# Performance work log

Hardware: AMD Instinct MI355X
Metric: run time of the kernel (lower is better)

The kernel has to match this reference:

```python
import jax, jax.numpy as jnp
import numpy as np

NUM_CLASS = 20
STRIDE = 4.0
B, H, W, G, NV = 8, 128, 128, 64, 40


def setup_inputs() -> dict:
    key = jax.random.key(0)
    ks = jax.random.split(key, 8)
    keypoints = jax.random.normal(ks[0], (B, H, W, NUM_CLASS), jnp.float32)
    preg = jax.random.uniform(ks[1], (B, H, W, 4), jnp.float32, 1.0, 40.0)
    fpn = jax.random.normal(ks[2], (B, H, W, NUM_CLASS), jnp.float32)
    masks = jnp.ones((B, H, W, G), jnp.float32)
    scalar_y = jax.random.uniform(ks[3], (B, G), jnp.float32, 5.0, 25.0)
    scalar_x = jax.random.uniform(ks[4], (B, G), jnp.float32, 5.0, 25.0)
    # ground truth: [cy, cx, y1, x1, y2, x2, class]; rows >= NV are zero padding
    rng = np.random.default_rng(0)
    gt = np.zeros((B, G, 7), np.float32)
    cy = rng.uniform(20.0, 492.0, (B, NV)).astype(np.float32)
    cx = rng.uniform(20.0, 492.0, (B, NV)).astype(np.float32)
    hh = rng.uniform(16.0, 120.0, (B, NV)).astype(np.float32)
    ww = rng.uniform(16.0, 120.0, (B, NV)).astype(np.float32)
    gt[:, :NV, 0] = cy
    gt[:, :NV, 1] = cx
    gt[:, :NV, 2] = np.clip(cy - hh / 2, 1.0, 510.0)
    gt[:, :NV, 3] = np.clip(cx - ww / 2, 1.0, 510.0)
    gt[:, :NV, 4] = np.clip(cy + hh / 2, 1.0, 510.0)
    gt[:, :NV, 5] = np.clip(cx + ww / 2, 1.0, 510.0)
    gt[:, :NV, 6] = rng.integers(1, NUM_CLASS + 1, (B, NV)).astype(np.float32)
    return {
        "keypoints": keypoints,
        "preg": preg,
        "fpn": fpn,
        "ground_truth": jnp.asarray(gt),
        "masks": masks,
        "scalar_y": scalar_y,
        "scalar_x": scalar_x,
    }


def _image_loss(gravity_pred, dist_pred, heatmap_pred, gt, masks, sy, sx):
    f32 = jnp.float32
    Hh, Ww, C = gravity_pred.shape
    Gg = gt.shape[0]
    # padding boundary: first row whose cy (col 0) is the minimum (==0 padding)
    slice_index = jnp.argmin(gt[:, 0])
    valid = jnp.arange(Gg) < slice_index
    vf = valid.astype(f32)

    gy = (gt[:, 0] + 0.5) / STRIDE
    gx = (gt[:, 1] + 0.5) / STRIDE
    by1 = (gt[:, 2] + 0.5) / STRIDE
    bx1 = (gt[:, 3] + 0.5) / STRIDE
    by2 = (gt[:, 4] + 0.5) / STRIDE
    bx2 = (gt[:, 5] + 0.5) / STRIDE
    cid = gt[:, 6].astype(jnp.int32) - 1
    kp_y = jnp.clip(jnp.floor(gt[:, 0] / STRIDE).astype(jnp.int32), 0, Hh - 1)
    kp_x = jnp.clip(jnp.floor(gt[:, 1] / STRIDE).astype(jnp.int32), 0, Ww - 1)

    grid_y = (jnp.arange(Hh, dtype=f32) + 0.5)[:, None, None]  # [H,1,1]
    grid_x = (jnp.arange(Ww, dtype=f32) + 0.5)[None, :, None]  # [1,W,1]

    dist_l = grid_x - bx1  # [1,W,G]
    dist_r = bx2 - grid_x
    dist_t = grid_y - by1  # [H,1,G]
    dist_b = by2 - grid_y
    ymask = (dist_t > 0.0).astype(f32) * (dist_b > 0.0).astype(f32)
    xmask = (dist_l > 0.0).astype(f32) * (dist_r > 0.0).astype(f32)
    heatmask = ymask * xmask * masks * vf  # [H,W,G]
    dist_l = dist_l * heatmask
    dist_r = dist_r * heatmask
    dist_t = dist_t * heatmask
    dist_b = dist_b * heatmask
    loc = jnp.max(heatmask, axis=-1)  # [H,W]
    dist_area = (dist_l + dist_r) * (dist_t + dist_b)
    area_pad = dist_area + (1.0 - heatmask) * 1e8
    area_min = jnp.min(area_pad, axis=-1, keepdims=True)
    dist_mask = (dist_area == area_min).astype(f32) * loc[..., None]  # [H,W,G]
    dl = jnp.max(dist_l * dist_mask, axis=-1)
    dr = jnp.max(dist_r * dist_mask, axis=-1)
    dt = jnp.max(dist_t * dist_mask, axis=-1)
    db = jnp.max(dist_b * dist_mask, axis=-1)

    pl, pr, pt, pb = (dist_pred[..., k] for k in range(4))
    inter = (jnp.minimum(dl, pl) + jnp.minimum(dr, pr)) * (jnp.minimum(dt, pt) + jnp.minimum(db, pb))
    union = (dl + dr) * (dt + db) + (pl + pr) * (pt + pb) - inter
    iou = inter / (union + 1e-12)

    red = jnp.exp(-(((grid_y - 0.5 - jnp.floor(gy)) / jnp.sqrt(sy)) ** 2
                    + ((grid_x - 0.5 - jnp.floor(gx)) / jnp.sqrt(sx)) ** 2) / 2.0) * vf  # [H,W,G]
    iou_red = jnp.max(red, axis=-1)
    iou_loss = jnp.sum(-jnp.log(iou + 1e-12) * loc * (iou_red * 4.0 + 1.0))

    # per-class max over gts of that class (== boolean_mask + reduce_max; empty -> 0)
    seg = jnp.where(valid & (cid >= 0) & (cid < C), cid, C)
    red_gt = jnp.maximum(jax.ops.segment_max(red.transpose(2, 0, 1), seg, num_segments=C + 1)[:C], 0.0).transpose(1, 2, 0)
    hm_gt = jnp.maximum(jax.ops.segment_max(dist_mask.transpose(2, 0, 1), seg, num_segments=C + 1)[:C], 0.0).transpose(1, 2, 0)
    gt_kp = jnp.zeros((Hh, Ww, C + 1), f32).at[kp_y, kp_x, seg].max(vf)[..., :C]

    sig, ls = jax.nn.sigmoid, jax.nn.log_sigmoid
    pos = -(1.0 - sig(gravity_pred)) ** 2 * ls(gravity_pred) * gt_kp
    neg = -(1.0 - red_gt) ** 4 * sig(gravity_pred) ** 2 * (-gravity_pred + ls(gravity_pred)) * (1.0 - gt_kp)
    gravity_loss = jnp.sum(pos) + jnp.sum(neg)

    hpos = -10.0 * (1.0 - sig(heatmap_pred)) ** 2 * ls(heatmap_pred) * hm_gt
    hneg = -10.0 * sig(heatmap_pred) ** 2 * (-heatmap_pred + ls(heatmap_pred)) * (1.0 - hm_gt)
    s_hg = jnp.sum(hm_gt)
    hm_loss = jnp.sum(hneg) / (jnp.asarray(Hh * Ww * C, f32) - s_hg)

    cond = s_hg != 0.0
    safe_hg = jnp.where(cond, s_hg, 1.0)
    s_loc = jnp.sum(loc)
    safe_loc = jnp.where(s_loc > 0.0, s_loc, 1.0)
    n_valid = jnp.maximum(slice_index.astype(f32), 1.0)
    hm2 = hm_loss + jnp.sum(hpos) / safe_hg
    iou_out = jnp.where(cond, iou_loss / safe_loc, 0.0)
    grav_out = jnp.where(cond, gravity_loss / n_valid, 0.0)
    hm_out = jnp.where(cond, hm2, hm_loss)
    total = jnp.where(cond, iou_out + grav_out + hm2, hm_loss)
    return iou_out, hm_out, grav_out, total


def reference(keypoints, preg, fpn, ground_truth, masks, scalar_y, scalar_x):
    losses = jax.vmap(_image_loss)(keypoints, preg, fpn, ground_truth, masks, scalar_y, scalar_x)
    # layer returns the mean total loss over the batch
    return jnp.mean(losses[3])
```

## Files before the change

### kernel.cpp

```cpp
#include <hip/hip_runtime.h>
#include <math.h>

#define Bc 8
#define Hc 128
#define Wc 128
#define Cc 20
#define Gc 64
#define HWc (Hc*Wc)
#define NBLK2 (Bc*HWc/128)

#define WS_STRIDE 768
#define OFF_BOX   0
#define OFF_RED   256
#define OFF_KPIX  512
#define OFF_SEG   576
#define OFF_START 640
#define WS_NV     704
#define WS_ACC    705
#define WS_SLICE  712

__global__ __launch_bounds__(64) void prep_kernel(
    const float* __restrict__ gt, const float* __restrict__ sy,
    const float* __restrict__ sx, float* __restrict__ ws)
{
  const int b = blockIdx.x;
  const int g = threadIdx.x;
  const float* row = gt + (size_t)(b*Gc + g)*7;
  const float cy = row[0];
  const float cx = row[1];

  float v = cy; int idx = g;
  #pragma unroll
  for (int o = 32; o > 0; o >>= 1) {
    const float ov = __shfl_down(v, o, 64);
    const int   oi = __shfl_down(idx, o, 64);
    if (ov < v || (ov == v && oi < idx)) { v = ov; idx = oi; }
  }
  const int slice = __shfl(idx, 0, 64);
  const bool valid = g < slice;
  const int cid = (int)row[6] - 1;
  const int cls = (cid >= 0 && cid < Cc) ? cid : Cc;

  __shared__ int counts[Cc+1], offs[Cc+1], starts[Cc+2];
  if (g < Cc+1) { counts[g] = 0; offs[g] = 0; }
  __syncthreads();
  if (valid) atomicAdd(&counts[cls], 1);
  __syncthreads();
  if (g == 0) {
    int acc = 0;
    for (int c = 0; c < Cc+1; ++c) { starts[c] = acc; acc += counts[c]; }
    starts[Cc+1] = acc;
  }
  __syncthreads();

  float* wb = ws + (size_t)b*WS_STRIDE;
  int*  wbi = (int*)wb;
  float4 bx;
  bx.x = (row[2]+0.5f)*0.25f;
  bx.y = (row[3]+0.5f)*0.25f;
  bx.z = (row[4]+0.5f)*0.25f;
  bx.w = (row[5]+0.5f)*0.25f;
  ((float4*)(wb + OFF_BOX))[g] = bx;
  wbi[OFF_SEG+g] = (valid && cls < Cc) ? cls : Cc;
  if (valid) {
    const int pos = starts[cls] + atomicAdd(&offs[cls], 1);
    float4 rp;
    rp.x = floorf((cy+0.5f)*0.25f);
    rp.y = floorf((cx+0.5f)*0.25f);
    rp.z = 0.5f / sy[b*Gc+g];
    rp.w = 0.5f / sx[b*Gc+g];
    ((float4*)(wb + OFF_RED))[pos] = rp;
    int kpy = (int)floorf(cy*0.25f); kpy = kpy < 0 ? 0 : (kpy > Hc-1 ? Hc-1 : kpy);
    int kpx = (int)floorf(cx*0.25f); kpx = kpx < 0 ? 0 : (kpx > Wc-1 ? Wc-1 : kpx);
    wbi[OFF_KPIX+pos] = kpy*Wc + kpx;
  }
  if (g < Cc+2) wbi[OFF_START+g] = starts[g];
  if (g == 0) { wb[WS_NV] = fmaxf((float)slice, 1.0f); wbi[WS_SLICE] = slice; }
  if (g < 6) wb[WS_ACC+g] = 0.0f;
}

__device__ __forceinline__ float wave_sum(float v) {
  #pragma unroll
  for (int o = 32; o > 0; o >>= 1) v += __shfl_down(v, o, 64);
  return v;
}

__global__ __launch_bounds__(256, 4) void main_kernel(
  const float* __restrict__ kpt, const float* __restrict__ preg,
  const float* __restrict__ fpn, const float* __restrict__ masks,
  const float* __restrict__ wsc, float* __restrict__ wsa)
{
  __shared__ float s_part[4][6];

  const int tid = threadIdx.x;
  const int wv = tid >> 6, ln = tid & 63;
  const int half = ln >> 5, sub = ln & 31;
  const int pi  = wv*32 + sub;
  const int pix = blockIdx.x*128 + pi;
  const int b   = blockIdx.x >> 7;
  const int hw  = pix & (HWc-1);
  const int h = hw >> 7, w = hw & (Wc-1);

  const float* wb  = wsc + (size_t)b*WS_STRIDE;
  const int*   wbi = (const int*)wb;
  const float4* __restrict__ box4 = (const float4*)(wb + OFF_BOX);
  const float4* __restrict__ red4 = (const float4*)(wb + OFF_RED);
  const int nslice = wbi[WS_SLICE];

  const float wx = w + 0.5f, hy = h + 0.5f;
  const float px_ = (float)w, py_ = (float)h;
  const float4* mrow4 = (const float4*)(masks + (size_t)pix*Gc);

  const float4 p4 = *(const float4*)(preg + (size_t)pix*4);
  const float4* kq4 = (const float4*)(kpt + (size_t)pix*Cc);
  const float4* fq4 = (const float4*)(fpn + (size_t)pix*Cc);
  const float4 kg0 = kq4[half], kg1 = kq4[2+half], kg2 = kq4[4];
  const float4 fg0 = fq4[half], fg1 = fq4[2+half], fg2 = fq4[4];

  float amin = 3.0e38f, loc = 0.f, mmin = 0.f; int gmin = 0;
  const int nC2 = (nslice + 7) >> 3;
  float4 mc0 = mrow4[half];
  float4 mc1 = mrow4[2 + half];
  for (int c2 = 0; c2 < nC2; ++c2) {
    const int pfci = 2*(c2+2) + half;
    const float4 mn = mrow4[pfci < 16 ? pfci : (14+half)];
    const int ci = 2*c2 + half;
    #pragma unroll
    for (int j = 0; j < 4; ++j) {
      const int g = ci*4 + j;
      const float m = (j==0)?mc0.x:(j==1)?mc0.y:(j==2)?mc0.z:mc0.w;
      const float4 bx = box4[g];
      const float dl = wx - bx.y, dr = bx.w - wx;
      const float dt = hy - bx.x, db = bx.z - hy;
      const bool inb = (dl > 0.f) & (dr > 0.f) & (dt > 0.f) & (db > 0.f)
                       & (g < nslice);
      const float hm = inb ? m : 0.f;
      const float area = (dl*hm + dr*hm) * (dt*hm + db*hm);
      const float ap = area + (1.f - hm)*1e8f;
      if (ap < amin) { amin = ap; gmin = g; mmin = m; }
      loc = fmaxf(loc, hm);
    }
    mc0 = mc1; mc1 = mn;
  }
  {
    const float o_amin = __shfl_xor(amin, 32, 64);
    const int   o_gmin = __shfl_xor(gmin, 32, 64);
    const float o_mmin = __shfl_xor(mmin, 32, 64);
    const float o_loc  = __shfl_xor(loc , 32, 64);
    if (o_amin < amin || (o_amin == amin && o_gmin < gmin)) {
      amin = o_amin; gmin = o_gmin; mmin = o_mmin;
    }
    loc = fmaxf(loc, o_loc);
  }

  float dlm=0.f, drm=0.f, dtm=0.f, dbm=0.f, hmval=0.f; int cmin = Cc;
  if (loc > 0.f) {
    const float4 bx = box4[gmin];
    const float dl = wx - bx.y, dr = bx.w - wx;
    const float dt = hy - bx.x, db = bx.z - hy;
    const float area = (dl*mmin + dr*mmin) * (dt*mmin + db*mmin);
    if (area == amin) {
      dlm = dl*mmin*loc; drm = dr*mmin*loc; dtm = dt*mmin*loc; dbm = db*mmin*loc;
      cmin = wbi[OFF_SEG + gmin];
      hmval = loc;
    }
  }

  float gargmax = -1e30f, grav = 0.f, hneg = 0.f;
  #pragma unroll
  for (int grp = 0; grp < 2; ++grp) {
    const int idx = 2*grp + half;
    const float4 kq = grp ? kg1 : kg0;
    const float4 fq = grp ? fg1 : fg0;
    #pragma unroll
    for (int j = 0; j < 4; ++j) {
      const int c = idx*4 + j;
      const int s0 = wbi[OFF_START + c];
      const int s1 = wbi[OFF_START + c + 1];
      float ramax = -1e30f; bool kpv = false;
      for (int i = s0; i < s1; ++i) {
        const float4 rp = red4[i];
        const int kpix = wbi[OFF_KPIX + i];
        const float dy = py_ - rp.x, dx = px_ - rp.y;
        const float arg = -(dy*dy*rp.z + dx*dx*rp.w);
        ramax = fmaxf(ramax, arg);
        kpv = kpv | (kpix == hw);
      }
      const float rmax = __expf(ramax);
      gargmax = fmaxf(gargmax, ramax);
      const float x  = (j==0)?kq.x:(j==1)?kq.y:(j==2)?kq.z:kq.w;
      const float e  = __expf(-fabsf(x));
      const float t  = 1.f + e;
      const float r  = 1.f / t;
      const float L  = __logf(t);
      const float s  = (x >= 0.f) ? r : e*r;
      const float lsx = fminf(x, 0.f) - L;
      const float kv = kpv ? 1.f : 0.f;
      const float om = 1.f - rmax;
      const float om4 = (om*om)*(om*om);
      const float oms = 1.f - s;
      grav += (-(oms*oms)*lsx)*kv + (-om4*(s*s)*(lsx - x))*(1.f - kv);

      const float fx  = (j==0)?fq.x:(j==1)?fq.y:(j==2)?fq.z:fq.w;
      const float ef  = __expf(-fabsf(fx));
      const float tf  = 1.f + ef;
      const float rf  = 1.f / tf;
      const float Lf  = __logf(tf);
      const float sf  = (fx >= 0.f) ? rf : ef*rf;
      const float lsf = fminf(fx, 0.f) - Lf;
      hneg += -10.f*(sf*sf)*(lsf - fx);
    }
  }
  #pragma unroll
  for (int j = 0; j < 2; ++j) {
    const int c = 16 + 2*half + j;
    const int cp = 2*half + j;
    const int s0 = wbi[OFF_START + c];
    const int s1 = wbi[OFF_START + c + 1];
    float ramax = -1e30f; bool kpv = false;
    for (int i = s0; i < s1; ++i) {
      const float4 rp = red4[i];
      const int kpix = wbi[OFF_KPIX + i];
      const float dy = py_ - rp.x, dx = px_ - rp.y;
      const float arg = -(dy*dy*rp.z + dx*dx*rp.w);
      ramax = fmaxf(ramax, arg);
      kpv = kpv | (kpix == hw);
    }
    const float rmax = __expf(ramax);
    gargmax = fmaxf(gargmax, ramax);
    const float x  = (cp==0)?kg2.x:(cp==1)?kg2.y:(cp==2)?kg2.z:kg2.w;
    const float e  = __expf(-fabsf(x));
    const float t  = 1.f + e;
    const float r  = 1.f / t;
    const float L  = __logf(t);
    const float s  = (x >= 0.f) ? r : e*r;
    const float lsx = fminf(x, 0.f) - L;
    const float kv = kpv ? 1.f : 0.f;
    const float om = 1.f - rmax;
    const float om4 = (om*om)*(om*om);
    const float oms = 1.f - s;
    grav += (-(oms*oms)*lsx)*kv + (-om4*(s*s)*(lsx - x))*(1.f - kv);

    const float fx  = (cp==0)?fg2.x:(cp==1)?fg2.y:(cp==2)?fg2.z:fg2.w;
    const float ef  = __expf(-fabsf(fx));
    const float tf  = 1.f + ef;
    const float rf  = 1.f / tf;
    const float Lf  = __logf(tf);
    const float sf  = (fx >= 0.f) ? rf : ef*rf;
    const float lsf = fminf(fx, 0.f) - Lf;
    hneg += -10.f*(sf*sf)*(lsf - fx);
  }
  if (half) {
    const int s0  = wbi[OFF_START + Cc];
    const int e20 = wbi[OFF_START + Cc + 1];
    for (int i = s0; i < e20; ++i) {
      const float4 rp = red4[i];
      const float dy = py_ - rp.x, dx = px_ - rp.y;
      gargmax = fmaxf(gargmax, -(dy*dy*rp.z + dx*dx*rp.w));
    }
  }
  gargmax = fmaxf(gargmax, __shfl_xor(gargmax, 32, 64));
  const float iou_red = __expf(gargmax);

  const float inter = (fminf(dlm,p4.x)+fminf(drm,p4.y)) * (fminf(dtm,p4.z)+fminf(dbm,p4.w));
  const float uni = (dlm+drm)*(dtm+dbm) + (p4.x+p4.y)*(p4.z+p4.w) - inter;
  const float iou = inter / (uni + 1e-12f);
  const float t_iou = -__logf(iou + 1e-12f) * loc * (iou_red*4.f + 1.f);

  float hpos = 0.f, shg = 0.f;
  if (half == 0 && hmval > 0.f && cmin < Cc) {
    const float fx  = fpn[(size_t)pix*Cc + cmin];
    const float ef  = __expf(-fabsf(fx));
    const float tf  = 1.f + ef;
    const float rf  = 1.f / tf;
    const float Lf  = __logf(tf);
    const float sf  = (fx >= 0.f) ? rf : ef*rf;
    const float lsf = fminf(fx, 0.f) - Lf;
    const float osf = 1.f - sf;
    hpos = -10.f*(osf*osf)*lsf*hmval;
    hneg -= (-10.f*(sf*sf)*(lsf - fx))*hmval;
    shg = hmval;
  }

  const float zi = half ? 0.f : 1.f;
  float v0 = wave_sum(t_iou * zi);
  float v1 = wave_sum(loc * zi);
  float v2 = wave_sum(grav);
  float v3 = wave_sum(hpos);
  float v4 = wave_sum(hneg);
  float v5 = wave_sum(shg);
  if (ln == 0) {
    s_part[wv][0]=v0; s_part[wv][1]=v1; s_part[wv][2]=v2;
    s_part[wv][3]=v3; s_part[wv][4]=v4; s_part[wv][5]=v5;
  }
  __syncthreads();
  if (tid < 6) {
    const float a = s_part[0][tid] + s_part[1][tid] + s_part[2][tid] + s_part[3][tid];
    atomicAdd(wsa + (size_t)b*WS_STRIDE + WS_ACC + tid, a);
  }
}

__global__ __launch_bounds__(64) void fin_kernel(const float* __restrict__ ws,
                                                 float* __restrict__ out)
{
  const int b = threadIdx.x;
  float total = 0.0f;
  if (b < Bc) {
    const float* wb = ws + (size_t)b*WS_STRIDE;
    const float iou_loss = wb[WS_ACC+0];
    const float s_loc    = wb[WS_ACC+1];
    const float grav     = wb[WS_ACC+2];
    const float hposs    = wb[WS_ACC+3];
    const float hnegs    = wb[WS_ACC+4];
    const float shg      = wb[WS_ACC+5];
    const float nv       = wb[WS_NV];
    const float hm_loss  = hnegs / ((float)(HWc*Cc) - shg);
    const bool  cond     = (shg != 0.0f);
    const float safe_hg  = cond ? shg : 1.0f;
    const float safe_loc = (s_loc > 0.0f) ? s_loc : 1.0f;
    const float hm2      = hm_loss + hposs/safe_hg;
    total = cond ? (iou_loss/safe_loc + grav/nv + hm2) : hm_loss;
  }
  #pragma unroll
  for (int o = 4; o > 0; o >>= 1) total += __shfl_down(total, o, 64);
  if (b == 0) out[0] = total * (1.0f/(float)Bc);
}

extern "C" void kernel_launch(void* const* d_in, const int* in_sizes, int n_in,
                              void* d_out, int out_size, void* d_ws, size_t ws_size,
                              hipStream_t stream) {
  const float* kpt  = (const float*)d_in[0];
  const float* preg = (const float*)d_in[1];
  const float* fpn  = (const float*)d_in[2];
  const float* gt   = (const float*)d_in[3];
  const float* mk   = (const float*)d_in[4];
  const float* sy   = (const float*)d_in[5];
  const float* sx   = (const float*)d_in[6];
  float* ws  = (float*)d_ws;
  float* out = (float*)d_out;

  prep_kernel<<<Bc, 64, 0, stream>>>(gt, sy, sx, ws);
  main_kernel<<<NBLK2, 256, 0, stream>>>(kpt, preg, fpn, mk, ws, ws);
  fin_kernel<<<1, 64, 0, stream>>>(ws, out);
}
```

Measured before the change: 119.8 us.

## Split pixel work across wave pairs instead of half-waves, exchange via LDS

Each pixel is now handled by two whole wavefronts (one per half of the boxes and classes) rather than two half-waves of the same wavefront. Partial min/argmin, loc and gargmax are combined through shared memory with a block barrier instead of cross-lane shuffles. Each wave now loads its masks as two contiguous float4s per step of an unrolled four-step loop, and class segment starts are carried forward instead of reloaded. This is meant to give contiguous per-lane memory access, but it adds LDS traffic, a __syncthreads, and leaves the second wave idle during the IoU tail.

New measurement: 120.2 us. No clear change (+0.4%).

```diff
diff --git a/kernel.cpp b/kernel.cpp
--- a/kernel.cpp
+++ b/kernel.cpp
@@ -7,7 +7,7 @@
 #define Cc 20
 #define Gc 64
 #define HWc (Hc*Wc)
-#define NBLK2 (Bc*HWc/128)
+#define NBLKM (Bc*HWc/128)
 
 #define WS_STRIDE 768
 #define OFF_BOX   0
@@ -91,11 +91,12 @@
   const float* __restrict__ wsc, float* __restrict__ wsa)
 {
   __shared__ float s_part[4][6];
+  __shared__ float s_ex[2][64][5];
 
   const int tid = threadIdx.x;
   const int wv = tid >> 6, ln = tid & 63;
-  const int half = ln >> 5, sub = ln & 31;
-  const int pi  = wv*32 + sub;
+  const int q = wv >> 1, hv = wv & 1;
+  const int pi  = q*64 + ln;
   const int pix = blockIdx.x*128 + pi;
   const int b   = blockIdx.x >> 7;
   const int hw  = pix & (HWc-1);
@@ -111,74 +112,56 @@
   const float px_ = (float)w, py_ = (float)h;
   const float4* mrow4 = (const float4*)(masks + (size_t)pix*Gc);
 
-  const float4 p4 = *(const float4*)(preg + (size_t)pix*4);
+  float4 p4 = make_float4(0.f,0.f,0.f,0.f);
+  if (hv == 0) p4 = *(const float4*)(preg + (size_t)pix*4);
   const float4* kq4 = (const float4*)(kpt + (size_t)pix*Cc);
   const float4* fq4 = (const float4*)(fpn + (size_t)pix*Cc);
-  const float4 kg0 = kq4[half], kg1 = kq4[2+half], kg2 = kq4[4];
-  const float4 fg0 = fq4[half], fg1 = fq4[2+half], fg2 = fq4[4];
+  const float4 kg0 = kq4[hv*2], kg1 = kq4[hv*2+1], kg2 = kq4[4];
+  const float4 fg0 = fq4[hv*2], fg1 = fq4[hv*2+1], fg2 = fq4[4];
+  float4 m0a = mrow4[2*hv],   m0b = mrow4[2*hv+1];
+  float4 m1a = mrow4[4+2*hv], m1b = mrow4[4+2*hv+1];
 
   float amin = 3.0e38f, loc = 0.f, mmin = 0.f; int gmin = 0;
-  const int nC2 = (nslice + 7) >> 3;
-  float4 mc0 = mrow4[half];
-  float4 mc1 = mrow4[2 + half];
-  for (int c2 = 0; c2 < nC2; ++c2) {
-    const int pfci = 2*(c2+2) + half;
-    const float4 mn = mrow4[pfci < 16 ? pfci : (14+half)];
-    const int ci = 2*c2 + half;
-    #pragma unroll
-    for (int j = 0; j < 4; ++j) {
-      const int g = ci*4 + j;
-      const float m = (j==0)?mc0.x:(j==1)?mc0.y:(j==2)?mc0.z:mc0.w;
-      const float4 bx = box4[g];
-      const float dl = wx - bx.y, dr = bx.w - wx;
-      const float dt = hy - bx.x, db = bx.z - hy;
-      const bool inb = (dl > 0.f) & (dr > 0.f) & (dt > 0.f) & (db > 0.f)
-                       & (g < nslice);
-      const float hm = inb ? m : 0.f;
-      const float area = (dl*hm + dr*hm) * (dt*hm + db*hm);
-      const float ap = area + (1.f - hm)*1e8f;
-      if (ap < amin) { amin = ap; gmin = g; mmin = m; }
-      loc = fmaxf(loc, hm);
-    }
-    mc0 = mc1; mc1 = mn;
-  }
-  {
-    const float o_amin = __shfl_xor(amin, 32, 64);
-    const int   o_gmin = __shfl_xor(gmin, 32, 64);
-    const float o_mmin = __shfl_xor(mmin, 32, 64);
-    const float o_loc  = __shfl_xor(loc , 32, 64);
-    if (o_amin < amin || (o_amin == amin && o_gmin < gmin)) {
-      amin = o_amin; gmin = o_gmin; mmin = o_mmin;
-    }
-    loc = fmaxf(loc, o_loc);
-  }
-
-  float dlm=0.f, drm=0.f, dtm=0.f, dbm=0.f, hmval=0.f; int cmin = Cc;
-  if (loc > 0.f) {
-    const float4 bx = box4[gmin];
-    const float dl = wx - bx.y, dr = bx.w - wx;
-    const float dt = hy - bx.x, db = bx.z - hy;
-    const float area = (dl*mmin + dr*mmin) * (dt*mmin + db*mmin);
-    if (area == amin) {
-      dlm = dl*mmin*loc; drm = dr*mmin*loc; dtm = dt*mmin*loc; dbm = db*mmin*loc;
-      cmin = wbi[OFF_SEG + gmin];
-      hmval = loc;
-    }
+  #pragma unroll
+  for (int c2 = 0; c2 < 4; ++c2) {
+    const int pfb = (c2 < 2) ? (4*(c2+2) + 2*hv) : (12 + 2*hv);
+    const float4 na = mrow4[pfb];
+    const float4 nb = mrow4[pfb + 1];
+    const int gbase = (2*c2 + hv)*8;
+    if (gbase < nslice) {
+      #pragma unroll
+      for (int j = 0; j < 8; ++j) {
+        const int g = gbase + j;
+        const float m = (j==0)?m0a.x:(j==1)?m0a.y:(j==2)?m0a.z:(j==3)?m0a.w
+                      : (j==4)?m0b.x:(j==5)?m0b.y:(j==6)?m0b.z:m0b.w;
+        const float4 bx = box4[g];
+        const float dl = wx - bx.y, dr = bx.w - wx;
+        const float dt = hy - bx.x, db = bx.z - hy;
+        const bool inb = (dl > 0.f) & (dr > 0.f) & (dt > 0.f) & (db > 0.f)
+                         & (g < nslice);
+        const float hm = inb ? m : 0.f;
+        const float area = (dl*hm + dr*hm) * (dt*hm + db*hm);
+        const float ap = area + (1.f - hm)*1e8f;
+        if (ap < amin) { amin = ap; gmin = g; mmin = m; }
+        loc = fmaxf(loc, hm);
+      }
+    }
+    m0a = m1a; m0b = m1b; m1a = na; m1b = nb;
   }
 
   float gargmax = -1e30f, grav = 0.f, hneg = 0.f;
+  const int cb = hv*8;
+  int sb = wbi[OFF_START + cb];
   #pragma unroll
   for (int grp = 0; grp < 2; ++grp) {
-    const int idx = 2*grp + half;
     const float4 kq = grp ? kg1 : kg0;
     const float4 fq = grp ? fg1 : fg0;
     #pragma unroll
     for (int j = 0; j < 4; ++j) {
-      const int c = idx*4 + j;
-      const int s0 = wbi[OFF_START + c];
+      const int c = cb + grp*4 + j;
       const int s1 = wbi[OFF_START + c + 1];
       float ramax = -1e30f; bool kpv = false;
-      for (int i = s0; i < s1; ++i) {
+      for (int i = sb; i < s1; ++i) {
         const float4 rp = red4[i];
         const int kpix = wbi[OFF_KPIX + i];
         const float dy = py_ - rp.x, dx = px_ - rp.y;
@@ -186,6 +169,7 @@
         ramax = fmaxf(ramax, arg);
         kpv = kpv | (kpix == hw);
       }
+      sb = s1;
       const float rmax = __expf(ramax);
       gargmax = fmaxf(gargmax, ramax);
       const float x  = (j==0)?kq.x:(j==1)?kq.y:(j==2)?kq.z:kq.w;
@@ -211,14 +195,14 @@
       hneg += -10.f*(sf*sf)*(lsf - fx);
     }
   }
+  sb = wbi[OFF_START + 16 + 2*hv];
   #pragma unroll
   for (int j = 0; j < 2; ++j) {
-    const int c = 16 + 2*half + j;
-    const int cp = 2*half + j;
-    const int s0 = wbi[OFF_START + c];
+    const int c  = 16 + 2*hv + j;
+    const int cp = 2*hv + j;
     const int s1 = wbi[OFF_START + c + 1];
     float ramax = -1e30f; bool kpv = false;
-    for (int i = s0; i < s1; ++i) {
+    for (int i = sb; i < s1; ++i) {
       const float4 rp = red4[i];
       const int kpix = wbi[OFF_KPIX + i];
       const float dy = py_ - rp.x, dx = px_ - rp.y;
@@ -226,6 +210,7 @@
       ramax = fmaxf(ramax, arg);
       kpv = kpv | (kpix == hw);
     }
+    sb = s1;
     const float rmax = __expf(ramax);
     gargmax = fmaxf(gargmax, ramax);
     const float x  = (cp==0)?kg2.x:(cp==1)?kg2.y:(cp==2)?kg2.z:kg2.w;
@@ -250,7 +235,7 @@
     const float lsf = fminf(fx, 0.f) - Lf;
     hneg += -10.f*(sf*sf)*(lsf - fx);
   }
-  if (half) {
+  if (hv) {
     const int s0  = wbi[OFF_START + Cc];
     const int e20 = wbi[OFF_START + Cc + 1];
     for (int i = s0; i < e20; ++i) {
@@ -259,32 +244,65 @@
       gargmax = fmaxf(gargmax, -(dy*dy*rp.z + dx*dx*rp.w));
     }
   }
-  gargmax = fmaxf(gargmax, __shfl_xor(gargmax, 32, 64));
-  const float iou_red = __expf(gargmax);
-
-  const float inter = (fminf(dlm,p4.x)+fminf(drm,p4.y)) * (fminf(dtm,p4.z)+fminf(dbm,p4.w));
-  const float uni = (dlm+drm)*(dtm+dbm) + (p4.x+p4.y)*(p4.z+p4.w) - inter;
-  const float iou = inter / (uni + 1e-12f);
-  const float t_iou = -__logf(iou + 1e-12f) * loc * (iou_red*4.f + 1.f);
-
-  float hpos = 0.f, shg = 0.f;
-  if (half == 0 && hmval > 0.f && cmin < Cc) {
-    const float fx  = fpn[(size_t)pix*Cc + cmin];
-    const float ef  = __expf(-fabsf(fx));
-    const float tf  = 1.f + ef;
-    const float rf  = 1.f / tf;
-    const float Lf  = __logf(tf);
-    const float sf  = (fx >= 0.f) ? rf : ef*rf;
-    const float lsf = fminf(fx, 0.f) - Lf;
-    const float osf = 1.f - sf;
-    hpos = -10.f*(osf*osf)*lsf*hmval;
-    hneg -= (-10.f*(sf*sf)*(lsf - fx))*hmval;
-    shg = hmval;
-  }
-
-  const float zi = half ? 0.f : 1.f;
-  float v0 = wave_sum(t_iou * zi);
-  float v1 = wave_sum(loc * zi);
+
+  if (hv) {
+    s_ex[q][ln][0] = amin;
+    s_ex[q][ln][1] = __int_as_float(gmin);
+    s_ex[q][ln][2] = mmin;
+    s_ex[q][ln][3] = loc;
+    s_ex[q][ln][4] = gargmax;
+  }
+  __syncthreads();
+
+  float t_iou = 0.f, locA = 0.f, hpos = 0.f, shg = 0.f;
+  if (hv == 0) {
+    const float o_amin = s_ex[q][ln][0];
+    const int   o_gmin = __float_as_int(s_ex[q][ln][1]);
+    const float o_mmin = s_ex[q][ln][2];
+    const float o_loc  = s_ex[q][ln][3];
+    gargmax = fmaxf(gargmax, s_ex[q][ln][4]);
+    if (o_amin < amin || (o_amin == amin && o_gmin < gmin)) {
+      amin = o_amin; gmin = o_gmin; mmin = o_mmin;
+    }
+    loc = fmaxf(loc, o_loc);
+    locA = loc;
+
+    float dlm=0.f, drm=0.f, dtm=0.f, dbm=0.f, hmval=0.f; int cmin = Cc;
+    if (loc > 0.f) {
+      const float4 bx = box4[gmin];
+      const float dl = wx - bx.y, dr = bx.w - wx;
+      const float dt = hy - bx.x, db = bx.z - hy;
+      const float area = (dl*mmin + dr*mmin) * (dt*mmin + db*mmin);
+      if (area == amin) {
+        dlm = dl*mmin*loc; drm = dr*mmin*loc; dtm = dt*mmin*loc; dbm = db*mmin*loc;
+        cmin = wbi[OFF_SEG + gmin];
+        hmval = loc;
+      }
+    }
+
+    const float iou_red = __expf(gargmax);
+    const float inter = (fminf(dlm,p4.x)+fminf(drm,p4.y)) * (fminf(dtm,p4.z)+fminf(dbm,p4.w));
+    const float uni = (dlm+drm)*(dtm+dbm) + (p4.x+p4.y)*(p4.z+p4.w) - inter;
+    const float iou = inter / (uni + 1e-12f);
+    t_iou = -__logf(iou + 1e-12f) * loc * (iou_red*4.f + 1.f);
+
+    if (hmval > 0.f && cmin < Cc) {
+      const float fx  = fpn[(size_t)pix*Cc + cmin];
+      const float ef  = __expf(-fabsf(fx));
+      const float tf  = 1.f + ef;
+      const float rf  = 1.f / tf;
+      const float Lf  = __logf(tf);
+      const float sf  = (fx >= 0.f) ? rf : ef*rf;
+      const float lsf = fminf(fx, 0.f) - Lf;
+      const float osf = 1.f - sf;
+      hpos = -10.f*(osf*osf)*lsf*hmval;
+      hneg -= (-10.f*(sf*sf)*(lsf - fx))*hmval;
+      shg = hmval;
+    }
+  }
+
+  float v0 = wave_sum(t_iou);
+  float v1 = wave_sum(locA);
   float v2 = wave_sum(grav);
   float v3 = wave_sum(hpos);
   float v4 = wave_sum(hneg);
@@ -340,6 +358,6 @@
   float* out = (float*)d_out;
 
   prep_kernel<<<Bc, 64, 0, stream>>>(gt, sy, sx, ws);
-  main_kernel<<<NBLK2, 256, 0, stream>>>(kpt, preg, fpn, mk, ws, ws);
+  main_kernel<<<NBLKM, 256, 0, stream>>>(kpt, preg, fpn, mk, ws, ws);
   fin_kernel<<<1, 64, 0, stream>>>(ws, out);
 }
```
